# Performance work log

Measured on AMD Instinct MI355X. Metric: run time of the kernel, lower is better.

The kernel has to match this reference:

```python
import jax, jax.numpy as jnp
import numpy as np

EPS = 1e-5
H, W, D_FULL, D_RFFT, DIM = 9, 11, 9, 5, 900  # spectral grid 9x11x9, rfft last dim -> 5

def layer_norm(x, gamma, beta):
    mu = jnp.mean(x, axis=-1, keepdims=True)
    var = jnp.var(x, axis=-1, keepdims=True)
    return (x - mu) * jax.lax.rsqrt(var + EPS) * gamma + beta

def setup_inputs() -> dict:
    key = jax.random.key(0)
    ks = jax.random.split(key, 12)
    B, N, C = 64, H * W * D_FULL, DIM  # N = 891
    hidden, rank = int(C * 2.0), C // 2  # 1800, 450
    return {
        "x": jax.random.normal(ks[0], (B, N, C), dtype=jnp.float32),
        # Global_Filter complex weight: (h, w, d, dim, 2), init ~ N(0,1)*0.02
        "cw": jax.random.normal(ks[1], (H, W, D_RFFT, C, 2), dtype=jnp.float32) * 0.02,
        "gamma1": jnp.ones((C,), jnp.float32),
        "beta1": jnp.zeros((C,), jnp.float32),
        "gamma2": jnp.ones((C,), jnp.float32),
        "beta2": jnp.zeros((C,), jnp.float32),
        # low-rank MLP (torch Linear weights are (out, in); we apply x @ W.T)
        "u1_w": jax.random.normal(ks[2], (rank, C), jnp.float32) * (1.0 / np.sqrt(C)),
        "v1_w": jax.random.normal(ks[3], (hidden, rank), jnp.float32) * (1.0 / np.sqrt(rank)),
        "v1_b": jnp.zeros((hidden,), jnp.float32),
        "u2_w": jax.random.normal(ks[4], (rank, hidden), jnp.float32) * (1.0 / np.sqrt(hidden)),
        "v2_w": jax.random.normal(ks[5], (C, rank), jnp.float32) * (1.0 / np.sqrt(rank)),
        "v2_b": jnp.zeros((C,), jnp.float32),
    }

def reference(x, cw, gamma1, beta1, gamma2, beta2, u1_w, v1_w, v1_b, u2_w, v2_w, v2_b):
    B, N, C = x.shape
    # norm1 -> global spectral filter
    y = layer_norm(x, gamma1, beta1)
    y = y.reshape(B, H, W, D_FULL, C)
    yf = jnp.fft.rfftn(y, axes=(1, 2, 3), norm="ortho")  # (B, 9, 11, 5, C) complex
    weight = jax.lax.complex(cw[..., 0], cw[..., 1])      # (9, 11, 5, C)
    yf = yf * weight
    y = jnp.fft.irfftn(yf, s=(H, W, D_FULL), axes=(1, 2, 3), norm="ortho")
    y = y.reshape(B, N, C)
    # norm2 -> low-rank MLP (dropout/droppath = identity in eval)
    z = layer_norm(y, gamma2, beta2)
    z = jnp.einsum("bnc,rc->bnr", z, u1_w)
    z = jnp.einsum("bnr,hr->bnh", z, v1_w) + v1_b
    z = jax.nn.gelu(z, approximate=False)
    z = jnp.einsum("bnh,rh->bnr", z, u2_w)
    z = jnp.einsum("bnr,cr->bnc", z, v2_w) + v2_b
    return x + z
```

## Files before the change

### kernel.cpp

```cpp
#include <hip/hip_runtime.h>


typedef unsigned short u16;
typedef __bf16 bf16x8 __attribute__((ext_vector_type(8)));
typedef float f32x4 __attribute__((ext_vector_type(4)));

#define LN_EPS 1e-5f

constexpr float KC9[9] = {
  1.0f, 0.766044443118978f, 0.17364817766693041f, -0.4999999999999998f,
  -0.9396926207859083f, -0.9396926207859084f, -0.5000000000000004f,
  0.17364817766692997f, 0.7660444431189778f };
constexpr float KS9[9] = {
  0.0f, 0.6427876096865393f, 0.984807753012208f, 0.8660254037844387f,
  0.3420201433256689f, -0.34202014332566866f, -0.8660254037844385f,
  -0.9848077530122081f, -0.6427876096865396f };
constexpr float KC11[11] = {
  1.0f, 0.8412535328311812f, 0.41541501300188644f, -0.14231483827328512f,
  -0.654860733945285f, -0.9594929736144974f, -0.9594929736144974f,
  -0.6548607339452852f, -0.14231483827328543f, 0.4154150130018863f,
  0.8412535328311811f };
constexpr float KS11[11] = {
  0.0f, 0.5406408174555976f, 0.9096319953545183f, 0.9898214418809327f,
  0.7557495743542583f, 0.2817325568414297f, -0.2817325568414296f,
  -0.7557495743542582f, -0.9898214418809327f, -0.9096319953545184f,
  -0.5406408174555979f };

__device__ __forceinline__ u16 f2bf(float f) {
  unsigned int u = __float_as_uint(f);
  return (u16)((u + 0x7fffu + ((u >> 16) & 1u)) >> 16);
}
__device__ __forceinline__ float gelu_f(float v) {
  return 0.5f * v * (1.f + erff(v * 0.70710678118654752440f));
}

__global__ __launch_bounds__(256) void k_cvt(const float* __restrict__ s, u16* __restrict__ d,
                                             int rows, int sc, int dc,
                                             const float* __restrict__ gamma) {
  int i = blockIdx.x * 256 + threadIdx.x;
  if (i >= rows * dc) return;
  int r = i / dc, c = i % dc;
  u16 o = 0;
  if (c < sc) {
    float v = s[(size_t)r * sc + c];
    if (gamma) v *= gamma[c];
    o = f2bf(v);
  }
  d[i] = o;
}

__global__ __launch_bounds__(256) void k_bias1(const float* __restrict__ u1w,
                                               const float* __restrict__ b2,
                                               float* __restrict__ out) {
  int r = blockIdx.x * 256 + threadIdx.x;
  if (r < 450) {
    float s = 0.f;
    for (int c = 0; c < 900; c++) s += u1w[r * 900 + c] * b2[c];
    out[r] = s;
  }
}

__global__ __launch_bounds__(256) void k_ln1_dfft(const float* __restrict__ x,
                                                  const float* __restrict__ g1,
                                                  const float* __restrict__ b1,
                                                  float* __restrict__ fre,
                                                  float* __restrict__ fim) {
  __shared__ float red1[9][256], red2[9][256];
  __shared__ float smu[9], srs[9];
  int blk = blockIdx.x;
  int t = threadIdx.x;
  const float* xb = x + (size_t)blk * 8100;

  float v[4][9], s1[9], s2[9];
#pragma unroll
  for (int d = 0; d < 9; d++) { s1[d] = 0.f; s2[d] = 0.f; }
#pragma unroll
  for (int i = 0; i < 4; i++) {
    int c = t + i * 256;
    bool ok = c < 900;
#pragma unroll
    for (int d = 0; d < 9; d++) {
      float a = ok ? xb[d * 900 + c] : 0.f;
      v[i][d] = a; s1[d] += a; s2[d] += a * a;
    }
  }
#pragma unroll
  for (int d = 0; d < 9; d++) { red1[d][t] = s1[d]; red2[d][t] = s2[d]; }
  __syncthreads();
  int w = t >> 6, l = t & 63;
  for (int d = w; d < 9; d += 4) {
    float p1 = red1[d][l] + red1[d][l + 64] + red1[d][l + 128] + red1[d][l + 192];
    float p2 = red2[d][l] + red2[d][l + 64] + red2[d][l + 128] + red2[d][l + 192];
#pragma unroll
    for (int off = 32; off > 0; off >>= 1) { p1 += __shfl_down(p1, off, 64); p2 += __shfl_down(p2, off, 64); }
    if (l == 0) {
      float m = p1 * (1.f / 900.f);
      float var = p2 * (1.f / 900.f) - m * m;
      smu[d] = m; srs[d] = rsqrtf(var + LN_EPS);
    }
  }
  __syncthreads();
  float mu[9], rs[9];
#pragma unroll
  for (int d = 0; d < 9; d++) { mu[d] = smu[d]; rs[d] = srs[d]; }

  size_t ob = (size_t)blk * 4500;
#pragma unroll
  for (int i = 0; i < 4; i++) {
    int c = t + i * 256;
    if (c < 900) {
      float g = g1[c], be = b1[c];
      float y[9];
#pragma unroll
      for (int d = 0; d < 9; d++) y[d] = (v[i][d] - mu[d]) * rs[d] * g + be;
#pragma unroll
      for (int kd = 0; kd < 5; kd++) {
        float re = 0.f, im = 0.f;
#pragma unroll
        for (int d = 0; d < 9; d++) { int j = (kd * d) % 9; re += y[d] * KC9[j]; im -= y[d] * KS9[j]; }
        fre[ob + (size_t)kd * 900 + c] = re;
        fim[ob + (size_t)kd * 900 + c] = im;
      }
    }
  }
}

template <int INV>
__global__ __launch_bounds__(256) void k_wfft(float* __restrict__ fre, float* __restrict__ fim) {
  int blk = blockIdx.x;
  int kd = blk % 5, bh = blk / 5;
  size_t base = (size_t)bh * 49500 + (size_t)kd * 900;
  int t = threadIdx.x;
  for (int c = t; c < 900; c += 256) {
    float xr[11], xi[11];
#pragma unroll
    for (int ww = 0; ww < 11; ww++) {
      size_t p = base + (size_t)ww * 4500 + c;
      xr[ww] = fre[p]; xi[ww] = fim[p];
    }
#pragma unroll
    for (int k = 0; k < 11; k++) {
      float yr = 0.f, yi = 0.f;
#pragma unroll
      for (int ww = 0; ww < 11; ww++) {
        int j = (k * ww) % 11;
        float cc = KC11[j], ss = KS11[j];
        if (INV) { yr += xr[ww] * cc - xi[ww] * ss; yi += xi[ww] * cc + xr[ww] * ss; }
        else     { yr += xr[ww] * cc + xi[ww] * ss; yi += xi[ww] * cc - xr[ww] * ss; }
      }
      size_t p = base + (size_t)k * 4500 + c;
      fre[p] = yr; fim[p] = yi;
    }
  }
}

__global__ __launch_bounds__(256) void k_hfilter(float* __restrict__ fre, float* __restrict__ fim,
                                                 const float* __restrict__ cw) {
  int blk = blockIdx.x;
  int b = blk / 55, r = blk % 55;
  size_t base = ((size_t)b * 495 + r) * 900;
  size_t wb = (size_t)r * 900;
  int t = threadIdx.x;
  for (int c = t; c < 900; c += 256) {
    float xr[9], xi[9];
#pragma unroll
    for (int h = 0; h < 9; h++) { size_t p = base + (size_t)h * 49500 + c; xr[h] = fre[p]; xi[h] = fim[p]; }
    float zr[9], zi[9];
#pragma unroll
    for (int k = 0; k < 9; k++) {
      float yr = 0.f, yi = 0.f;
#pragma unroll
      for (int h = 0; h < 9; h++) {
        int j = (k * h) % 9; float cc = KC9[j], ss = KS9[j];
        yr += xr[h] * cc + xi[h] * ss;
        yi += xi[h] * cc - xr[h] * ss;
      }
      size_t widx = (wb + (size_t)k * 49500 + c) * 2;
      float wr = cw[widx], wim = cw[widx + 1];
      zr[k] = yr * wr - yi * wim;
      zi[k] = yr * wim + yi * wr;
    }
#pragma unroll
    for (int h = 0; h < 9; h++) {
      float orr = 0.f, oi = 0.f;
#pragma unroll
      for (int k = 0; k < 9; k++) {
        int j = (k * h) % 9; float cc = KC9[j], ss = KS9[j];
        orr += zr[k] * cc - zi[k] * ss;
        oi  += zi[k] * cc + zr[k] * ss;
      }
      size_t p = base + (size_t)h * 49500 + c;
      fre[p] = orr; fim[p] = oi;
    }
  }
}

__global__ __launch_bounds__(256) void k_difft_ln2(const float* __restrict__ fre,
                                                   const float* __restrict__ fim,
                                                   u16* __restrict__ yn) {
  __shared__ float red1[9][256], red2[9][256];
  __shared__ float smu[9], srs[9];
  int blk = blockIdx.x;
  int t = threadIdx.x;
  size_t ib = (size_t)blk * 4500;

  float v[4][9], s1[9], s2[9];
#pragma unroll
  for (int d = 0; d < 9; d++) { s1[d] = 0.f; s2[d] = 0.f; }
#pragma unroll
  for (int i = 0; i < 4; i++) {
    int c = t + i * 256;
    bool ok = c < 900;
    int cc = ok ? c : 0;
    float Xr[5], Xi[5];
#pragma unroll
    for (int k = 0; k < 5; k++) { size_t p = ib + (size_t)k * 900 + cc; Xr[k] = fre[p]; Xi[k] = fim[p]; }
#pragma unroll
    for (int d = 0; d < 9; d++) {
      float acc = Xr[0];
#pragma unroll
      for (int k = 1; k < 5; k++) { int j = (k * d) % 9; acc += 2.f * (Xr[k] * KC9[j] - Xi[k] * KS9[j]); }
      acc *= (1.f / 891.f);
      if (!ok) acc = 0.f;
      v[i][d] = acc; s1[d] += acc; s2[d] += acc * acc;
    }
  }
#pragma unroll
  for (int d = 0; d < 9; d++) { red1[d][t] = s1[d]; red2[d][t] = s2[d]; }
  __syncthreads();
  int w = t >> 6, l = t & 63;
  for (int d = w; d < 9; d += 4) {
    float p1 = red1[d][l] + red1[d][l + 64] + red1[d][l + 128] + red1[d][l + 192];
    float p2 = red2[d][l] + red2[d][l + 64] + red2[d][l + 128] + red2[d][l + 192];
#pragma unroll
    for (int off = 32; off > 0; off >>= 1) { p1 += __shfl_down(p1, off, 64); p2 += __shfl_down(p2, off, 64); }
    if (l == 0) {
      float m = p1 * (1.f / 900.f);
      float var = p2 * (1.f / 900.f) - m * m;
      smu[d] = m; srs[d] = rsqrtf(var + LN_EPS);
    }
  }
  __syncthreads();
  float mu[9], rs[9];
#pragma unroll
  for (int d = 0; d < 9; d++) { mu[d] = smu[d]; rs[d] = srs[d]; }

  size_t tok0 = (size_t)blk * 9;
#pragma unroll
  for (int i = 0; i < 4; i++) {
    int c = t + i * 256;
    if (c < 900) {
#pragma unroll
      for (int d = 0; d < 9; d++)
        yn[(tok0 + d) * 928 + c] = f2bf((v[i][d] - mu[d]) * rs[d]);
    }
  }
  if (t < 28) {
#pragma unroll
    for (int d = 0; d < 9; d++) yn[(tok0 + d) * 928 + 900 + t] = 0;
  }
}

typedef __attribute__((address_space(1))) void gvoid;
typedef __attribute__((address_space(3))) void svoid;

__device__ __forceinline__ void stage16(const u16* g, u16* lbase, int lane) {
#if __has_builtin(__builtin_amdgcn_global_load_lds)
  __builtin_amdgcn_global_load_lds((gvoid*)(void*)g, (svoid*)lbase, 16, 0, 0);
#else
  *(uint4*)(lbase + lane * 8) = *(const uint4*)g;
#endif
}

template <int EPI>
__global__ __launch_bounds__(256, 2) void k_gemm(
    const u16* __restrict__ A, const u16* __restrict__ B,
    int M, int N, int Kt, int ldk, int NT,
    u16* __restrict__ Ob, int ldo, int Nstore,
    const float* __restrict__ bias,
    const float* __restrict__ Xres, float* __restrict__ Of) {
  __shared__ u16 As[128 * 32];
  __shared__ u16 Bs[128 * 32];
  int t = threadIdx.x, w = t >> 6, l = t & 63;
  int mt = blockIdx.x / NT, nt = blockIdx.x % NT;
  int m0 = mt * 128, n0 = nt * 128;
  int arow = (w << 4) + (l >> 2);
  int koff = (l & 3) * 8;
  int wm = (w >> 1) << 6, wn = (w & 1) << 6;
  int fr = l & 15, fq = l >> 4;

  f32x4 acc[4][4];
  f32x4 zero = {0.f, 0.f, 0.f, 0.f};
#pragma unroll
  for (int i = 0; i < 4; i++)
#pragma unroll
    for (int j = 0; j < 4; j++) acc[i][j] = zero;

  for (int kt = 0; kt < Kt; ++kt) {
    int k0 = kt * 32;
#pragma unroll
    for (int j = 0; j < 2; j++) {
      int r = (j << 6) + arow;
      int gm = m0 + r; gm = gm < M ? gm : M - 1;
      stage16(A + (size_t)gm * ldk + (k0 + koff), &As[((j << 6) + (w << 4)) * 32], l);
      int gn = n0 + r; gn = gn < N ? gn : N - 1;
      stage16(B + (size_t)gn * ldk + (k0 + koff), &Bs[((j << 6) + (w << 4)) * 32], l);
    }
    __syncthreads();
    bf16x8 af[4], bfr[4];
#pragma unroll
    for (int i = 0; i < 4; i++) af[i] = *(const bf16x8*)&As[(wm + (i << 4) + fr) * 32 + fq * 8];
#pragma unroll
    for (int i = 0; i < 4; i++) bfr[i] = *(const bf16x8*)&Bs[(wn + (i << 4) + fr) * 32 + fq * 8];
#pragma unroll
    for (int i = 0; i < 4; i++)
#pragma unroll
      for (int j = 0; j < 4; j++)
        acc[i][j] = __builtin_amdgcn_mfma_f32_16x16x32_bf16(af[i], bfr[j], acc[i][j], 0, 0, 0);
    __syncthreads();
  }

#pragma unroll
  for (int j = 0; j < 4; j++) {
    int gn = n0 + wn + (j << 4) + fr;
    float bv = 0.f;
    if (EPI != 2) bv = (gn < Nstore) ? bias[gn] : 0.f;
#pragma unroll
    for (int i = 0; i < 4; i++) {
#pragma unroll
      for (int r = 0; r < 4; r++) {
        int gm = m0 + wm + (i << 4) + (fq << 2) + r;
        if (gm < M) {
          float val = acc[i][j][r] + bv;
          if (EPI == 1) val = gelu_f(val);
          if (EPI == 3) {
            if (gn < Nstore) Of[(size_t)gm * Nstore + gn] = val + Xres[(size_t)gm * Nstore + gn];
          } else {
            if (gn < ldo) Ob[(size_t)gm * ldo + gn] = (gn < Nstore) ? f2bf(val) : (u16)0;
          }
        }
      }
    }
  }
}

extern "C" void kernel_launch(void* const* d_in, const int* in_sizes, int n_in,
                              void* d_out, int out_size, void* d_ws, size_t ws_size,
                              hipStream_t stream) {
  const float* x   = (const float*)d_in[0];
  const float* cw  = (const float*)d_in[1];
  const float* g1  = (const float*)d_in[2];
  const float* b1  = (const float*)d_in[3];
  const float* g2  = (const float*)d_in[4];
  const float* b2  = (const float*)d_in[5];
  const float* u1w = (const float*)d_in[6];
  const float* v1w = (const float*)d_in[7];
  const float* v1b = (const float*)d_in[8];
  const float* u2w = (const float*)d_in[9];
  const float* v2w = (const float*)d_in[10];
  const float* v2b = (const float*)d_in[11];

  char* ws = (char*)d_ws;
  float* fre = (float*)ws;
  float* fim = (float*)(ws + 114048000);
  u16*   t2  = (u16*)ws;
  u16*   t3  = (u16*)(ws + 228096000);
  u16*   u1g = (u16*)(ws + 286488576);
  u16*   v1c = (u16*)(ws + 287323776);
  u16*   u2c = (u16*)(ws + 289166976);
  u16*   v2c = (u16*)(ws + 290808576);
  float* b1r = (float*)(ws + 291730176);

  u16*   yn  = (u16*)d_out;
  u16*   t1  = (u16*)((char*)d_out + 105836544);
  float* outF = (float*)d_out;

  k_cvt<<<1632, 256, 0, stream>>>(u1w, u1g, 450, 900, 928, g2);
  k_cvt<<<3600, 256, 0, stream>>>(v1w, v1c, 1800, 450, 512, nullptr);
  k_cvt<<<3207, 256, 0, stream>>>(u2w, u2c, 450, 1800, 1824, nullptr);
  k_cvt<<<1800, 256, 0, stream>>>(v2w, v2c, 900, 450, 512, nullptr);
  k_bias1<<<2, 256, 0, stream>>>(u1w, b2, b1r);

  k_ln1_dfft<<<6336, 256, 0, stream>>>(x, g1, b1, fre, fim);
  k_wfft<0><<<2880, 256, 0, stream>>>(fre, fim);
  k_hfilter<<<3520, 256, 0, stream>>>(fre, fim, cw);
  k_wfft<1><<<2880, 256, 0, stream>>>(fre, fim);
  k_difft_ln2<<<6336, 256, 0, stream>>>(fre, fim, yn);

  k_gemm<0><<<446 * 4,  256, 0, stream>>>(yn, u1g, 57024, 450,  29, 928,  4,  t1, 512, 450, b1r, nullptr, nullptr);
  k_gemm<1><<<446 * 15, 256, 0, stream>>>(t1, v1c, 57024, 1800, 16, 512,  15, t2, 1824, 1800, v1b, nullptr, nullptr);
  k_gemm<2><<<446 * 4,  256, 0, stream>>>(t2, u2c, 57024, 450,  57, 1824, 4,  t3, 512, 450, nullptr, nullptr, nullptr);
  k_gemm<3><<<446 * 8,  256, 0, stream>>>(t3, v2c, 57024, 900,  16, 512,  8,  nullptr, 0, 900, v2b, x, outF);
}
```

Before: 1.610 ms.

## Fuse spectral filter passes into one LDS-resident kernel per channel chunk

```diff
diff --git a/kernel.cpp b/kernel.cpp
--- a/kernel.cpp
+++ b/kernel.cpp
@@ -6,6 +6,7 @@
 typedef float f32x4 __attribute__((ext_vector_type(4)));
 
 #define LN_EPS 1e-5f
+#define CH 16
 
 constexpr float KC9[9] = {
   1.0f, 0.766044443118978f, 0.17364817766693041f, -0.4999999999999998f,
@@ -31,7 +32,10 @@
   return (u16)((u + 0x7fffu + ((u >> 16) & 1u)) >> 16);
 }
 __device__ __forceinline__ float gelu_f(float v) {
-  return 0.5f * v * (1.f + erff(v * 0.70710678118654752440f));
+  float t = 0.7978845608028654f * v * (1.f + 0.044715f * v * v);
+  float e = __expf(2.f * t);
+  float th = 1.f - 2.f * __builtin_amdgcn_rcpf(e + 1.f);
+  return 0.5f * v * (1.f + th);
 }
 
 __global__ __launch_bounds__(256) void k_cvt(const float* __restrict__ s, u16* __restrict__ d,
@@ -60,204 +64,181 @@
   }
 }
 
-__global__ __launch_bounds__(256) void k_ln1_dfft(const float* __restrict__ x,
+__global__ __launch_bounds__(256) void k_stats1(const float* __restrict__ x,
+                                                float2* __restrict__ stats) {
+  int tok = blockIdx.x * 4 + (threadIdx.x >> 6);
+  int l = threadIdx.x & 63;
+  const float* row = x + (size_t)tok * 900;
+  float s1 = 0.f, s2 = 0.f;
+#pragma unroll
+  for (int j = 0; j < 15; j++) {
+    int c = l + j * 64;
+    if (c < 900) { float a = row[c]; s1 += a; s2 += a * a; }
+  }
+#pragma unroll
+  for (int off = 32; off; off >>= 1) { s1 += __shfl_xor(s1, off, 64); s2 += __shfl_xor(s2, off, 64); }
+  if (l == 0) {
+    float m = s1 * (1.f / 900.f);
+    float var = s2 * (1.f / 900.f) - m * m;
+    stats[tok] = make_float2(m, rsqrtf(var + LN_EPS));
+  }
+}
+
+__global__ __launch_bounds__(256) void k_spectral(const float* __restrict__ x,
+                                                  const float2* __restrict__ stats,
                                                   const float* __restrict__ g1,
                                                   const float* __restrict__ b1,
-                                                  float* __restrict__ fre,
-                                                  float* __restrict__ fim) {
-  __shared__ float red1[9][256], red2[9][256];
-  __shared__ float smu[9], srs[9];
-  int blk = blockIdx.x;
+                                                  const float* __restrict__ cw,
+                                                  float* __restrict__ y) {
+  __shared__ float sre[5 * 99 * CH];
+  __shared__ float sim[5 * 99 * CH];
+  int b = blockIdx.x / 57, cc = blockIdx.x % 57;
+  int c0 = cc * CH;
   int t = threadIdx.x;
-  const float* xb = x + (size_t)blk * 8100;
-
-  float v[4][9], s1[9], s2[9];
-#pragma unroll
-  for (int d = 0; d < 9; d++) { s1[d] = 0.f; s2[d] = 0.f; }
-#pragma unroll
-  for (int i = 0; i < 4; i++) {
-    int c = t + i * 256;
-    bool ok = c < 900;
+  const float* xb = x + (size_t)b * 801900;
+  const float2* st = stats + (size_t)b * 891;
+
+  for (int col = t; col < 99 * CH; col += 256) {
+    int pos = col / CH, c = col % CH;
+    int cg = c0 + c; bool ok = cg < 900;
+    float g = ok ? g1[cg] : 0.f, be = ok ? b1[cg] : 0.f;
+    float yv[9];
 #pragma unroll
     for (int d = 0; d < 9; d++) {
-      float a = ok ? xb[d * 900 + c] : 0.f;
-      v[i][d] = a; s1[d] += a; s2[d] += a * a;
-    }
-  }
-#pragma unroll
-  for (int d = 0; d < 9; d++) { red1[d][t] = s1[d]; red2[d][t] = s2[d]; }
+      float a = ok ? xb[(size_t)(pos * 9 + d) * 900 + cg] : 0.f;
+      float2 s = st[pos * 9 + d];
+      yv[d] = (a - s.x) * s.y * g + be;
+    }
+#pragma unroll
+    for (int kd = 0; kd < 5; kd++) {
+      float re = 0.f, im = 0.f;
+#pragma unroll
+      for (int d = 0; d < 9; d++) { int j = (kd * d) % 9; re += yv[d] * KC9[j]; im -= yv[d] * KS9[j]; }
+      sre[(kd * 99 + pos) * CH + c] = re;
+      sim[(kd * 99 + pos) * CH + c] = im;
+    }
+  }
   __syncthreads();
-  int w = t >> 6, l = t & 63;
-  for (int d = w; d < 9; d += 4) {
-    float p1 = red1[d][l] + red1[d][l + 64] + red1[d][l + 128] + red1[d][l + 192];
-    float p2 = red2[d][l] + red2[d][l + 64] + red2[d][l + 128] + red2[d][l + 192];
-#pragma unroll
-    for (int off = 32; off > 0; off >>= 1) { p1 += __shfl_down(p1, off, 64); p2 += __shfl_down(p2, off, 64); }
-    if (l == 0) {
-      float m = p1 * (1.f / 900.f);
-      float var = p2 * (1.f / 900.f) - m * m;
-      smu[d] = m; srs[d] = rsqrtf(var + LN_EPS);
-    }
-  }
-  __syncthreads();
-  float mu[9], rs[9];
-#pragma unroll
-  for (int d = 0; d < 9; d++) { mu[d] = smu[d]; rs[d] = srs[d]; }
-
-  size_t ob = (size_t)blk * 4500;
-#pragma unroll
-  for (int i = 0; i < 4; i++) {
-    int c = t + i * 256;
-    if (c < 900) {
-      float g = g1[c], be = b1[c];
-      float y[9];
-#pragma unroll
-      for (int d = 0; d < 9; d++) y[d] = (v[i][d] - mu[d]) * rs[d] * g + be;
-#pragma unroll
-      for (int kd = 0; kd < 5; kd++) {
-        float re = 0.f, im = 0.f;
-#pragma unroll
-        for (int d = 0; d < 9; d++) { int j = (kd * d) % 9; re += y[d] * KC9[j]; im -= y[d] * KS9[j]; }
-        fre[ob + (size_t)kd * 900 + c] = re;
-        fim[ob + (size_t)kd * 900 + c] = im;
-      }
-    }
-  }
-}
-
-template <int INV>
-__global__ __launch_bounds__(256) void k_wfft(float* __restrict__ fre, float* __restrict__ fim) {
-  int blk = blockIdx.x;
-  int kd = blk % 5, bh = blk / 5;
-  size_t base = (size_t)bh * 49500 + (size_t)kd * 900;
-  int t = threadIdx.x;
-  for (int c = t; c < 900; c += 256) {
+
+  for (int col = t; col < 5 * 9 * CH; col += 256) {
+    int kd = col / (9 * CH), r = col % (9 * CH), h = r / CH, c = r % CH;
+    int base = (kd * 99 + h * 11) * CH + c;
     float xr[11], xi[11];
 #pragma unroll
-    for (int ww = 0; ww < 11; ww++) {
-      size_t p = base + (size_t)ww * 4500 + c;
-      xr[ww] = fre[p]; xi[ww] = fim[p];
-    }
+    for (int w = 0; w < 11; w++) { xr[w] = sre[base + w * CH]; xi[w] = sim[base + w * CH]; }
 #pragma unroll
     for (int k = 0; k < 11; k++) {
       float yr = 0.f, yi = 0.f;
 #pragma unroll
-      for (int ww = 0; ww < 11; ww++) {
-        int j = (k * ww) % 11;
-        float cc = KC11[j], ss = KS11[j];
-        if (INV) { yr += xr[ww] * cc - xi[ww] * ss; yi += xi[ww] * cc + xr[ww] * ss; }
-        else     { yr += xr[ww] * cc + xi[ww] * ss; yi += xi[ww] * cc - xr[ww] * ss; }
-      }
-      size_t p = base + (size_t)k * 4500 + c;
-      fre[p] = yr; fim[p] = yi;
-    }
-  }
-}
-
-__global__ __launch_bounds__(256) void k_hfilter(float* __restrict__ fre, float* __restrict__ fim,
-                                                 const float* __restrict__ cw) {
-  int blk = blockIdx.x;
-  int b = blk / 55, r = blk % 55;
-  size_t base = ((size_t)b * 495 + r) * 900;
-  size_t wb = (size_t)r * 900;
-  int t = threadIdx.x;
-  for (int c = t; c < 900; c += 256) {
+      for (int w = 0; w < 11; w++) {
+        int j = (k * w) % 11; float cf = KC11[j], sf = KS11[j];
+        yr += xr[w] * cf + xi[w] * sf;
+        yi += xi[w] * cf - xr[w] * sf;
+      }
+      sre[base + k * CH] = yr; sim[base + k * CH] = yi;
+    }
+  }
+  __syncthreads();
+
+  for (int col = t; col < 5 * 11 * CH; col += 256) {
+    int kd = col / (11 * CH), r = col % (11 * CH), kw = r / CH, c = r % CH;
+    int cg = c0 + c;
+    int base = (kd * 99 + kw) * CH + c;
     float xr[9], xi[9];
 #pragma unroll
-    for (int h = 0; h < 9; h++) { size_t p = base + (size_t)h * 49500 + c; xr[h] = fre[p]; xi[h] = fim[p]; }
+    for (int h = 0; h < 9; h++) { xr[h] = sre[base + h * 11 * CH]; xi[h] = sim[base + h * 11 * CH]; }
     float zr[9], zi[9];
 #pragma unroll
     for (int k = 0; k < 9; k++) {
       float yr = 0.f, yi = 0.f;
 #pragma unroll
       for (int h = 0; h < 9; h++) {
-        int j = (k * h) % 9; float cc = KC9[j], ss = KS9[j];
-        yr += xr[h] * cc + xi[h] * ss;
-        yi += xi[h] * cc - xr[h] * ss;
-      }
-      size_t widx = (wb + (size_t)k * 49500 + c) * 2;
-      float wr = cw[widx], wim = cw[widx + 1];
-      zr[k] = yr * wr - yi * wim;
-      zi[k] = yr * wim + yi * wr;
+        int j = (k * h) % 9; float cf = KC9[j], sf = KS9[j];
+        yr += xr[h] * cf + xi[h] * sf;
+        yi += xi[h] * cf - xr[h] * sf;
+      }
+      float wr = 0.f, wi = 0.f;
+      if (cg < 900) {
+        size_t widx = ((size_t)((k * 11 + kw) * 5 + kd) * 900 + cg) * 2;
+        wr = cw[widx]; wi = cw[widx + 1];
+      }
+      zr[k] = yr * wr - yi * wi;
+      zi[k] = yr * wi + yi * wr;
     }
 #pragma unroll
     for (int h = 0; h < 9; h++) {
       float orr = 0.f, oi = 0.f;
 #pragma unroll
       for (int k = 0; k < 9; k++) {
-        int j = (k * h) % 9; float cc = KC9[j], ss = KS9[j];
-        orr += zr[k] * cc - zi[k] * ss;
-        oi  += zi[k] * cc + zr[k] * ss;
-      }
-      size_t p = base + (size_t)h * 49500 + c;
-      fre[p] = orr; fim[p] = oi;
-    }
-  }
-}
-
-__global__ __launch_bounds__(256) void k_difft_ln2(const float* __restrict__ fre,
-                                                   const float* __restrict__ fim,
-                                                   u16* __restrict__ yn) {
-  __shared__ float red1[9][256], red2[9][256];
-  __shared__ float smu[9], srs[9];
-  int blk = blockIdx.x;
-  int t = threadIdx.x;
-  size_t ib = (size_t)blk * 4500;
-
-  float v[4][9], s1[9], s2[9];
-#pragma unroll
-  for (int d = 0; d < 9; d++) { s1[d] = 0.f; s2[d] = 0.f; }
-#pragma unroll
-  for (int i = 0; i < 4; i++) {
-    int c = t + i * 256;
-    bool ok = c < 900;
-    int cc = ok ? c : 0;
+        int j = (k * h) % 9; float cf = KC9[j], sf = KS9[j];
+        orr += zr[k] * cf - zi[k] * sf;
+        oi  += zi[k] * cf + zr[k] * sf;
+      }
+      sre[base + h * 11 * CH] = orr; sim[base + h * 11 * CH] = oi;
+    }
+  }
+  __syncthreads();
+
+  for (int col = t; col < 5 * 9 * CH; col += 256) {
+    int kd = col / (9 * CH), r = col % (9 * CH), h = r / CH, c = r % CH;
+    int base = (kd * 99 + h * 11) * CH + c;
+    float xr[11], xi[11];
+#pragma unroll
+    for (int w = 0; w < 11; w++) { xr[w] = sre[base + w * CH]; xi[w] = sim[base + w * CH]; }
+#pragma unroll
+    for (int k = 0; k < 11; k++) {
+      float yr = 0.f, yi = 0.f;
+#pragma unroll
+      for (int w = 0; w < 11; w++) {
+        int j = (k * w) % 11; float cf = KC11[j], sf = KS11[j];
+        yr += xr[w] * cf - xi[w] * sf;
+        yi += xi[w] * cf + xr[w] * sf;
+      }
+      sre[base + k * CH] = yr; sim[base + k * CH] = yi;
+    }
+  }
+  __syncthreads();
+
+  for (int col = t; col < 99 * CH; col += 256) {
+    int pos = col / CH, c = col % CH;
+    int cg = c0 + c;
+    if (cg >= 900) continue;
     float Xr[5], Xi[5];
 #pragma unroll
-    for (int k = 0; k < 5; k++) { size_t p = ib + (size_t)k * 900 + cc; Xr[k] = fre[p]; Xi[k] = fim[p]; }
+    for (int k = 0; k < 5; k++) { Xr[k] = sre[(k * 99 + pos) * CH + c]; Xi[k] = sim[(k * 99 + pos) * CH + c]; }
 #pragma unroll
     for (int d = 0; d < 9; d++) {
       float acc = Xr[0];
 #pragma unroll
       for (int k = 1; k < 5; k++) { int j = (k * d) % 9; acc += 2.f * (Xr[k] * KC9[j] - Xi[k] * KS9[j]); }
-      acc *= (1.f / 891.f);
-      if (!ok) acc = 0.f;
-      v[i][d] = acc; s1[d] += acc; s2[d] += acc * acc;
-    }
-  }
-#pragma unroll
-  for (int d = 0; d < 9; d++) { red1[d][t] = s1[d]; red2[d][t] = s2[d]; }
-  __syncthreads();
-  int w = t >> 6, l = t & 63;
-  for (int d = w; d < 9; d += 4) {
-    float p1 = red1[d][l] + red1[d][l + 64] + red1[d][l + 128] + red1[d][l + 192];
-    float p2 = red2[d][l] + red2[d][l + 64] + red2[d][l + 128] + red2[d][l + 192];
-#pragma unroll
-    for (int off = 32; off > 0; off >>= 1) { p1 += __shfl_down(p1, off, 64); p2 += __shfl_down(p2, off, 64); }
-    if (l == 0) {
-      float m = p1 * (1.f / 900.f);
-      float var = p2 * (1.f / 900.f) - m * m;
-      smu[d] = m; srs[d] = rsqrtf(var + LN_EPS);
-    }
-  }
-  __syncthreads();
-  float mu[9], rs[9];
-#pragma unroll
-  for (int d = 0; d < 9; d++) { mu[d] = smu[d]; rs[d] = srs[d]; }
-
-  size_t tok0 = (size_t)blk * 9;
-#pragma unroll
-  for (int i = 0; i < 4; i++) {
-    int c = t + i * 256;
-    if (c < 900) {
-#pragma unroll
-      for (int d = 0; d < 9; d++)
-        yn[(tok0 + d) * 928 + c] = f2bf((v[i][d] - mu[d]) * rs[d]);
-    }
-  }
-  if (t < 28) {
-#pragma unroll
-    for (int d = 0; d < 9; d++) yn[(tok0 + d) * 928 + 900 + t] = 0;
+      y[((size_t)b * 891 + pos * 9 + d) * 900 + cg] = acc * (1.f / 891.f);
+    }
+  }
+}
+
+__global__ __launch_bounds__(256) void k_ln2(const float* __restrict__ y, u16* __restrict__ yn) {
+  int tok = blockIdx.x * 4 + (threadIdx.x >> 6);
+  int l = threadIdx.x & 63;
+  const float* row = y + (size_t)tok * 900;
+  float v[15];
+  float s1 = 0.f, s2 = 0.f;
+#pragma unroll
+  for (int j = 0; j < 15; j++) {
+    int c = l + j * 64;
+    float a = (c < 900) ? row[c] : 0.f;
+    v[j] = a; s1 += a; s2 += a * a;
+  }
+#pragma unroll
+  for (int off = 32; off; off >>= 1) { s1 += __shfl_xor(s1, off, 64); s2 += __shfl_xor(s2, off, 64); }
+  float m = s1 * (1.f / 900.f);
+  float var = s2 * (1.f / 900.f) - m * m;
+  float rs = rsqrtf(var + LN_EPS);
+  u16* orow = yn + (size_t)tok * 928;
+#pragma unroll
+  for (int j = 0; j < 15; j++) {
+    int c = l + j * 64;
+    if (c < 900) orow[c] = f2bf((v[j] - m) * rs);
+    else if (c < 928) orow[c] = 0;
   }
 }
 
@@ -361,8 +342,7 @@
   const float* v2b = (const float*)d_in[11];
 
   char* ws = (char*)d_ws;
-  float* fre = (float*)ws;
-  float* fim = (float*)(ws + 114048000);
+  float* y   = (float*)ws;
   u16*   t2  = (u16*)ws;
   u16*   t3  = (u16*)(ws + 228096000);
   u16*   u1g = (u16*)(ws + 286488576);
@@ -371,9 +351,10 @@
   u16*   v2c = (u16*)(ws + 290808576);
   float* b1r = (float*)(ws + 291730176);
 
-  u16*   yn  = (u16*)d_out;
-  u16*   t1  = (u16*)((char*)d_out + 105836544);
-  float* outF = (float*)d_out;
+  u16*    yn    = (u16*)d_out;
+  u16*    t1    = (u16*)((char*)d_out + 105836544);
+  float2* stats = (float2*)((char*)d_out + 164229120);
+  float*  outF  = (float*)d_out;
 
   k_cvt<<<1632, 256, 0, stream>>>(u1w, u1g, 450, 900, 928, g2);
   k_cvt<<<3600, 256, 0, stream>>>(v1w, v1c, 1800, 450, 512, nullptr);
@@ -381,11 +362,9 @@
   k_cvt<<<1800, 256, 0, stream>>>(v2w, v2c, 900, 450, 512, nullptr);
   k_bias1<<<2, 256, 0, stream>>>(u1w, b2, b1r);
 
-  k_ln1_dfft<<<6336, 256, 0, stream>>>(x, g1, b1, fre, fim);
-  k_wfft<0><<<2880, 256, 0, stream>>>(fre, fim);
-  k_hfilter<<<3520, 256, 0, stream>>>(fre, fim, cw);
-  k_wfft<1><<<2880, 256, 0, stream>>>(fre, fim);
-  k_difft_ln2<<<6336, 256, 0, stream>>>(fre, fim, yn);
+  k_stats1<<<14256, 256, 0, stream>>>(x, stats);
+  k_spectral<<<64 * 57, 256, 0, stream>>>(x, stats, g1, b1, cw, y);
+  k_ln2<<<14256, 256, 0, stream>>>(y, yn);
 
   k_gemm<0><<<446 * 4,  256, 0, stream>>>(yn, u1g, 57024, 450,  29, 928,  4,  t1, 512, 450, b1r, nullptr, nullptr);
   k_gemm<1><<<446 * 15, 256, 0, stream>>>(t1, v1c, 57024, 1800, 16, 512,  15, t2, 1824, 1800, v1b, nullptr, nullptr);
```

Result: faster. 1.496 ms (-7.1%).
